# Kernel optimization log

Hardware: AMD Instinct MI355X
Metric: run time of the kernel (lower is better)

The kernel has to match this reference:

```python
import jax, jax.numpy as jnp
import numpy as np

B, S, D, H, F, L, V = 8, 512, 768, 12, 3072, 12, 30522
DK = D // H
SCALE = 1.0 / float(np.sqrt(DK))


def _ln(x, g, b, eps):
    mu = jnp.mean(x, -1, keepdims=True)
    var = jnp.mean((x - mu) ** 2, -1, keepdims=True)
    return (x - mu) / jnp.sqrt(var + eps) * g + b


def setup_inputs() -> dict:
    key = jax.random.key(0)
    ks = jax.random.split(key, 16)
    s = 0.02
    d = {
        'input_ids': jax.random.randint(ks[0], (B, S), 0, V),
        'token_type_ids': jax.random.randint(ks[1], (B, S), 0, 2),
        'attention_mask': jnp.ones((B, S), jnp.float32),
        'word_emb': jax.random.normal(ks[2], (V, D), jnp.float32) * s,
        'pos_emb': jax.random.normal(ks[3], (512, D), jnp.float32) * s,
        'type_emb': jax.random.normal(ks[4], (2, D), jnp.float32) * s,
        'emb_ln_g': jnp.ones((D,), jnp.float32),
        'emb_ln_b': jnp.zeros((D,), jnp.float32),
        # per-layer stacked params (torch Linear convention: W is [out,in])
        'Wq': jax.random.normal(ks[5], (L, D, D), jnp.float32) * s,
        'bq': jnp.zeros((L, D), jnp.float32),
        'Wk': jax.random.normal(ks[6], (L, D, D), jnp.float32) * s,
        'bk': jnp.zeros((L, D), jnp.float32),
        'Wv': jax.random.normal(ks[7], (L, D, D), jnp.float32) * s,
        'bv': jnp.zeros((L, D), jnp.float32),
        'Wo': jax.random.normal(ks[8], (L, D, D), jnp.float32) * s,
        'bo': jnp.zeros((L, D), jnp.float32),
        'attn_ln_g': jnp.ones((L, D), jnp.float32),
        'attn_ln_b': jnp.zeros((L, D), jnp.float32),
        'W1': jax.random.normal(ks[9], (L, F, D), jnp.float32) * s,
        'b1': jnp.zeros((L, F), jnp.float32),
        'W2': jax.random.normal(ks[10], (L, D, F), jnp.float32) * s,
        'b2': jnp.zeros((L, D), jnp.float32),
        'ffn_ln_g': jnp.ones((L, D), jnp.float32),
        'ffn_ln_b': jnp.zeros((L, D), jnp.float32),
    }
    return d


def reference(input_ids, token_type_ids, attention_mask, word_emb, pos_emb,
              type_emb, emb_ln_g, emb_ln_b, Wq, bq, Wk, bk, Wv, bv, Wo, bo,
              attn_ln_g, attn_ln_b, W1, b1, W2, b2, ffn_ln_g, ffn_ln_b):
    # Embeddings (dropout = identity in eval)
    x = word_emb[input_ids] + type_emb[token_type_ids] + pos_emb[:S][None]
    x = _ln(x, emb_ln_g, emb_ln_b, 1e-12)

    mask0 = attention_mask[:, None, None, :] == 0  # (B,1,1,S)

    def step(x, p):
        wq, bq_, wk, bk_, wv, bv_, wo, bo_, ag, ab, w1, b1_, w2, b2_, fg, fb = p
        q = (jnp.einsum('bsd,ed->bse', x, wq) + bq_).reshape(B, S, H, DK).transpose(0, 2, 1, 3)
        k = (jnp.einsum('bsd,ed->bse', x, wk) + bk_).reshape(B, S, H, DK).transpose(0, 2, 1, 3)
        v = (jnp.einsum('bsd,ed->bse', x, wv) + bv_).reshape(B, S, H, DK).transpose(0, 2, 1, 3)
        attn = jnp.einsum('bhqd,bhkd->bhqk', q, k) * SCALE  # (B,H,S,S)
        attn = jnp.where(mask0, -1e9, attn)
        p_attn = jax.nn.softmax(attn, axis=-1)
        ctx = jnp.einsum('bhqk,bhkd->bhqd', p_attn, v).transpose(0, 2, 1, 3).reshape(B, S, D)
        a = _ln(jnp.einsum('bsd,ed->bse', ctx, wo) + bo_ + x, ag, ab, 1e-5)
        # FFN: NO activation, and final LN has NO residual (faithful to source)
        h = jnp.einsum('bsd,fd->bsf', a, w1) + b1_
        y = jnp.einsum('bsf,df->bsd', h, w2) + b2_
        return _ln(y, fg, fb, 1e-5), None

    x, _ = jax.lax.scan(step, x, (Wq, bq, Wk, bk, Wv, bv, Wo, bo,
                                  attn_ln_g, attn_ln_b, W1, b1, W2, b2,
                                  ffn_ln_g, ffn_ln_b))
    return x
```

## Files before the change

### kernel.cpp

```cpp
#include <hip/hip_runtime.h>
#include <hip/hip_bf16.h>
#include <cstdint>
#include <cstddef>

typedef __bf16 bf16;
typedef __bf16 bf16x8 __attribute__((ext_vector_type(8)));
typedef __bf16 bf16x4 __attribute__((ext_vector_type(4)));
typedef float  floatx4 __attribute__((ext_vector_type(4)));

__device__ __forceinline__ void gload_lds16(const bf16* g, bf16* l) {
    __builtin_amdgcn_global_load_lds((const __attribute__((address_space(1))) void*)g,
                                     (__attribute__((address_space(3))) void*)l, 16, 0, 0);
}

__device__ __forceinline__ floatx4 mfma16(bf16x8 a, bf16x8 b, floatx4 c) {
    return __builtin_amdgcn_mfma_f32_16x16x32_bf16(a, b, c, 0, 0, 0);
}

template<int MODE, int TN, int SPLITK>
__global__ __launch_bounds__(256)
void gemm_bt(const bf16* __restrict__ A, const bf16* __restrict__ Bw,
             const float* __restrict__ bias0, const float* __restrict__ bias1,
             const float* __restrict__ bias2,
             float* __restrict__ Cf, float* __restrict__ Cf1,
             bf16* __restrict__ Cb0, bf16* __restrict__ Cb1,
             bf16* __restrict__ Cb2,
             int M, int N, int K)
{
    constexpr int NJ  = TN / 32;
    constexpr int ASZ = 128 * 32;
    constexpr int BSZ = TN * 32;
    __shared__ __attribute__((aligned(16))) bf16 As[2 * ASZ];
    __shared__ __attribute__((aligned(16))) bf16 Bs[2 * BSZ];

    const int tid  = threadIdx.x;
    const int lane = tid & 63;
    const int wv   = tid >> 6;
    const int quad = lane >> 4;
    const int l16  = lane & 15;

    int bx = blockIdx.x, by = blockIdx.y;
    {
        const int nwg = gridDim.x * gridDim.y;
        if ((nwg & 7) == 0) {
            int wg = by * gridDim.x + bx;
            wg = (wg & 7) * (nwg >> 3) + (wg >> 3);
            bx = wg % gridDim.x;
            by = wg / gridDim.x;
        }
    }
    const int m0 = by * 128;
    const int n0 = bx * TN;
    const int wm = wv & 1;
    const int wn = wv >> 1;

    const int kz   = (SPLITK > 1) ? blockIdx.z : 0;
    const int Ksub = K / SPLITK;

    floatx4 acc[4][NJ] = {};

    const int srow = lane >> 2;
    const int scol = (lane & 3) * 8;
    const bf16* gA0 = A  + (size_t)(m0 + wv * 16 + srow) * K + kz * Ksub + scol;
    const bf16* gA1 = gA0 + (size_t)64 * K;
    const bf16* gB0 = Bw + (size_t)(n0 + wv * 16 + srow) * K + kz * Ksub + scol;
    const bf16* gB1 = gB0 + (size_t)64 * K;
    bf16* lA0 = &As[wv * 512];
    bf16* lA1 = &As[2048 + wv * 512];
    bf16* lB0 = &Bs[wv * 512];
    bf16* lB1 = &Bs[2048 + wv * 512];

    auto stage = [&](int k0, int bi) {
        gload_lds16(gA0 + k0, lA0 + bi * ASZ);
        gload_lds16(gA1 + k0, lA1 + bi * ASZ);
        gload_lds16(gB0 + k0, lB0 + bi * BSZ);
        if (TN == 128) gload_lds16(gB1 + k0, lB1 + bi * BSZ);
    };

    stage(0, 0);
    int cur = 0;
    for (int k0 = 0; k0 < Ksub; k0 += 32) {
        __syncthreads();
        if (k0 + 32 < Ksub) stage(k0 + 32, cur ^ 1);

        const bf16* Ab = &As[cur * ASZ];
        const bf16* Bb = &Bs[cur * BSZ];
        bf16x8 af[4], bfr[NJ];
        #pragma unroll
        for (int i = 0; i < 4; ++i)
            af[i] = *(const bf16x8*)&Ab[(wm * 64 + i * 16 + l16) * 32 + quad * 8];
        #pragma unroll
        for (int j = 0; j < NJ; ++j)
            bfr[j] = *(const bf16x8*)&Bb[(wn * NJ * 16 + j * 16 + l16) * 32 + quad * 8];

        #pragma unroll
        for (int i = 0; i < 4; ++i)
            #pragma unroll
            for (int j = 0; j < NJ; ++j)
                acc[i][j] = mfma16(af[i], bfr[j], acc[i][j]);
        cur ^= 1;
    }

    float* dstF = (SPLITK > 1 && kz != 0) ? Cf1 : Cf;

    #pragma unroll
    for (int i = 0; i < 4; ++i) {
        const int rbase = m0 + wm * 64 + i * 16 + quad * 4;
        #pragma unroll
        for (int j = 0; j < NJ; ++j) {
            const int col = n0 + wn * NJ * 16 + j * 16 + l16;
            if (MODE == 0) {
                const float bv = (SPLITK > 1 && kz != 0) ? 0.f : bias0[col];
                #pragma unroll
                for (int r = 0; r < 4; ++r)
                    dstF[(size_t)(rbase + r) * N + col] = acc[i][j][r] + bv;
            } else if (MODE == 1) {
                const float bv = bias0[col];
                #pragma unroll
                for (int r = 0; r < 4; ++r)
                    Cb0[(size_t)(rbase + r) * N + col] = (bf16)(acc[i][j][r] + bv);
            } else {
                const int sel = col / 768;
                const int cc  = col - sel * 768;
                if (sel < 2) {
                    bf16* dst = (sel == 0) ? Cb0 : Cb1;
                    const float bv = ((sel == 0) ? bias0 : bias1)[cc];
                    #pragma unroll
                    for (int r = 0; r < 4; ++r)
                        dst[(size_t)(rbase + r) * 768 + cc] = (bf16)(acc[i][j][r] + bv);
                } else {
                    const float bv = bias2[cc];
                    const int bb = rbase >> 9, s = rbase & 511;
                    const int h = cc >> 6, d = cc & 63;
                    bf16x4 o;
                    #pragma unroll
                    for (int r = 0; r < 4; ++r) o[r] = (bf16)(acc[i][j][r] + bv);
                    *(bf16x4*)(Cb2 + (((size_t)(bb * 12 + h) * 64 + d) * 512 + s)) = o;
                }
            }
        }
    }
}

__global__ __launch_bounds__(256)
void cvt_all(const float* __restrict__ Wq, const float* __restrict__ Wk,
             const float* __restrict__ Wv, const float* __restrict__ Wo,
             const float* __restrict__ W1, const float* __restrict__ W2,
             bf16* __restrict__ out)
{
    const int l = blockIdx.y;
    const size_t i = ((size_t)blockIdx.x * 256 + threadIdx.x) * 4;
    const size_t wdd = 589824, wdf = 2359296;
    const float* src;
    size_t off;
    if      (i <  589824) { src = Wq + l * wdd; off = i; }
    else if (i < 1179648) { src = Wk + l * wdd; off = i - 589824; }
    else if (i < 1769472) { src = Wv + l * wdd; off = i - 1179648; }
    else if (i < 2359296) { src = Wo + l * wdd; off = i - 1769472; }
    else if (i < 4718592) { src = W1 + l * wdf; off = i - 2359296; }
    else                  { src = W2 + l * wdf; off = i - 4718592; }
    const float4 v = *(const float4*)(src + off);
    bf16x4 o;
    o[0] = (bf16)v.x; o[1] = (bf16)v.y; o[2] = (bf16)v.z; o[3] = (bf16)v.w;
    *(bf16x4*)(out + (size_t)l * 7077888 + i) = o;
}

__global__ __launch_bounds__(256)
void attn3(const bf16* __restrict__ Q, const bf16* __restrict__ Kb,
           const bf16* __restrict__ VT, const float* __restrict__ mask,
           bf16* __restrict__ CTX)
{
    __shared__ __attribute__((aligned(16))) bf16 Ks[2][64 * 64];
    __shared__ __attribute__((aligned(16))) bf16 Vs[2][64 * 64];
    __shared__ __attribute__((aligned(16))) bf16 Ps[4 * 16 * 72];
    __shared__ float mb[512];

    const int tid  = threadIdx.x;
    const int lane = tid & 63;
    const int w    = tid >> 6;
    const int quad = lane >> 4;
    const int l16  = lane & 15;
    const int qt = blockIdx.x, h = blockIdx.y, b = blockIdx.z;

    mb[tid]       = (mask[b * 512 + tid] == 0.f)       ? -1e9f : -16.0f;
    mb[tid + 256] = (mask[b * 512 + tid + 256] == 0.f) ? -1e9f : -16.0f;

    bf16x8 qf0, qf1;
    {
        const bf16* qp = Q + (size_t)(b * 512 + qt * 64 + w * 16 + l16) * 768 + h * 64;
        qf0 = *(const bf16x8*)(qp + quad * 8);
        qf1 = *(const bf16x8*)(qp + 32 + quad * 8);
    }

    float lsum[4] = {0.f, 0.f, 0.f, 0.f};
    floatx4 accO[4] = {};
    bf16* pw = &Ps[w * 1152];

    const int srow8 = lane >> 3;
    const int scol8 = ((lane & 7) * 8) ^ (srow8 << 3);
    const int r0b   = w * 16;

    auto stageKV = [&](int kt, int bi) {
        #pragma unroll
        for (int i = 0; i < 2; ++i) {
            const int r0 = r0b + i * 8;
            gload_lds16(Kb + (size_t)(b * 512 + kt * 64 + r0 + srow8) * 768 + h * 64 + scol8,
                        &Ks[bi][r0 * 64]);
            gload_lds16(VT + ((size_t)(b * 12 + h) * 64 + r0 + srow8) * 512 + kt * 64 + scol8,
                        &Vs[bi][r0 * 64]);
        }
    };

    stageKV(0, 0);
    int cur = 0;
    const int swm = (l16 & 7) << 3;

    for (int kt = 0; kt < 8; ++kt) {
        __syncthreads();
        if (kt < 7) stageKV(kt + 1, cur ^ 1);

        #pragma unroll
        for (int ct = 0; ct < 4; ++ct) {
            const bf16x8 kf0 = *(const bf16x8*)&Ks[cur][(ct * 16 + l16) * 64 + ((quad * 8) ^ swm)];
            const bf16x8 kf1 = *(const bf16x8*)&Ks[cur][(ct * 16 + l16) * 64 + ((quad * 8 + 32) ^ swm)];
            floatx4 a = {0.f, 0.f, 0.f, 0.f};
            a = mfma16(qf0, kf0, a);
            a = mfma16(qf1, kf1, a);
            const float mbv = mb[kt * 64 + ct * 16 + l16];
            #pragma unroll
            for (int r = 0; r < 4; ++r) {
                const float p = __expf(fmaf(a[r], 0.125f, mbv));
                lsum[r] += p;
                pw[(quad * 4 + r) * 72 + ct * 16 + l16] = (bf16)p;
            }
        }

        #pragma unroll
        for (int kc = 0; kc < 2; ++kc) {
            const bf16x8 af = *(const bf16x8*)&pw[l16 * 72 + kc * 32 + quad * 8];
            #pragma unroll
            for (int ct2 = 0; ct2 < 4; ++ct2) {
                const bf16x8 bv = *(const bf16x8*)&Vs[cur][(ct2 * 16 + l16) * 64 + ((kc * 32 + quad * 8) ^ swm)];
                accO[ct2] = mfma16(af, bv, accO[ct2]);
            }
        }
        cur ^= 1;
    }

    float inv[4];
    #pragma unroll
    for (int r = 0; r < 4; ++r) {
        float s = lsum[r];
        #pragma unroll
        for (int o = 1; o < 16; o <<= 1) s += __shfl_xor(s, o);
        inv[r] = 1.0f / s;
    }
    #pragma unroll
    for (int ct2 = 0; ct2 < 4; ++ct2)
        #pragma unroll
        for (int r = 0; r < 4; ++r) {
            const int row = qt * 64 + w * 16 + quad * 4 + r;
            CTX[(size_t)(b * 512 + row) * 768 + h * 64 + ct2 * 16 + l16] =
                (bf16)(accO[ct2][r] * inv[r]);
        }
}

__global__ __launch_bounds__(256)
void embed_ln_k(const int* __restrict__ ids, const int* __restrict__ tts,
                const float* __restrict__ we, const float* __restrict__ pe,
                const float* __restrict__ te, const float* __restrict__ g,
                const float* __restrict__ b, float* __restrict__ X,
                bf16* __restrict__ XB)
{
    __shared__ float red[4];
    const int row = blockIdx.x;
    const int s   = row & 511;
    const int tid = threadIdx.x;
    const int id  = ids[row];
    const int tt  = tts[row];
    const float* pwp = we + (size_t)id * 768;
    const float* pt = te + (size_t)tt * 768;
    const float* pp = pe + (size_t)s * 768;
    const size_t base = (size_t)row * 768;

    float v[3];
    #pragma unroll
    for (int j = 0; j < 3; ++j) {
        const int c = tid + j * 256;
        v[j] = pwp[c] + pt[c] + pp[c];
    }
    float sm = v[0] + v[1] + v[2];
    for (int o = 32; o; o >>= 1) sm += __shfl_down(sm, o);
    if ((tid & 63) == 0) red[tid >> 6] = sm;
    __syncthreads();
    const float mu = (red[0] + red[1] + red[2] + red[3]) * (1.0f / 768.0f);
    float q = 0.f;
    #pragma unroll
    for (int j = 0; j < 3; ++j) { const float d = v[j] - mu; q += d * d; }
    __syncthreads();
    for (int o = 32; o; o >>= 1) q += __shfl_down(q, o);
    if ((tid & 63) == 0) red[tid >> 6] = q;
    __syncthreads();
    const float var  = (red[0] + red[1] + red[2] + red[3]) * (1.0f / 768.0f);
    const float rstd = rsqrtf(var + 1e-12f);
    #pragma unroll
    for (int j = 0; j < 3; ++j) {
        const int c = tid + j * 256;
        const float o = (v[j] - mu) * rstd * g[c] + b[c];
        X[base + c]  = o;
        XB[base + c] = (bf16)o;
    }
}

__global__ __launch_bounds__(256)
void ln_k(const float* T, const float* T2, const float* res,
          const float* g, const float* bta,
          float* Xo, bf16* XBo)
{
    __shared__ float red[4];
    const int row = blockIdx.x;
    const int tid = threadIdx.x;
    const size_t base = (size_t)row * 768;

    float v[3];
    #pragma unroll
    for (int j = 0; j < 3; ++j) {
        const int c = tid + j * 256;
        float x = T[base + c];
        if (T2)  x += T2[base + c];
        if (res) x += res[base + c];
        v[j] = x;
    }
    float sm = v[0] + v[1] + v[2];
    for (int o = 32; o; o >>= 1) sm += __shfl_down(sm, o);
    if ((tid & 63) == 0) red[tid >> 6] = sm;
    __syncthreads();
    const float mu = (red[0] + red[1] + red[2] + red[3]) * (1.0f / 768.0f);
    float q = 0.f;
    #pragma unroll
    for (int j = 0; j < 3; ++j) { const float d = v[j] - mu; q += d * d; }
    __syncthreads();
    for (int o = 32; o; o >>= 1) q += __shfl_down(q, o);
    if ((tid & 63) == 0) red[tid >> 6] = q;
    __syncthreads();
    const float var  = (red[0] + red[1] + red[2] + red[3]) * (1.0f / 768.0f);
    const float rstd = rsqrtf(var + 1e-5f);
    #pragma unroll
    for (int j = 0; j < 3; ++j) {
        const int c = tid + j * 256;
        const float o = (v[j] - mu) * rstd * g[c] + bta[c];
        Xo[base + c]  = o;
        XBo[base + c] = (bf16)o;
    }
}

extern "C" void kernel_launch(void* const* d_in, const int* in_sizes, int n_in,
                              void* d_out, int out_size, void* d_ws, size_t ws_size,
                              hipStream_t stream)
{
    const int*   ids  = (const int*)d_in[0];
    const int*   tts  = (const int*)d_in[1];
    const float* mask = (const float*)d_in[2];
    const float* wemb = (const float*)d_in[3];
    const float* pemb = (const float*)d_in[4];
    const float* temb = (const float*)d_in[5];
    const float* eg   = (const float*)d_in[6];
    const float* eb   = (const float*)d_in[7];
    const float* Wq   = (const float*)d_in[8];
    const float* bq   = (const float*)d_in[9];
    const float* Wk   = (const float*)d_in[10];
    const float* bk   = (const float*)d_in[11];
    const float* Wv   = (const float*)d_in[12];
    const float* bv   = (const float*)d_in[13];
    const float* Wo   = (const float*)d_in[14];
    const float* bo   = (const float*)d_in[15];
    const float* ag   = (const float*)d_in[16];
    const float* ab   = (const float*)d_in[17];
    const float* W1   = (const float*)d_in[18];
    const float* b1   = (const float*)d_in[19];
    const float* W2   = (const float*)d_in[20];
    const float* b2   = (const float*)d_in[21];
    const float* fg   = (const float*)d_in[22];
    const float* fb   = (const float*)d_in[23];

    char* p = (char*)d_ws;
    float* X   = (float*)p; p += 12582912;
    bf16* XB   = (bf16*)p;  p += 6291456;
    bf16* Qb   = (bf16*)p;  p += 6291456;
    bf16* Kbuf = (bf16*)p;  p += 6291456;
    bf16* CTXb = (bf16*)p;  p += 6291456;
    float* T1  = (float*)p; p += 12582912;
    bf16* HB   = (bf16*)p;  p += 25165824;
    bf16* WB   = (bf16*)p;  p += 169869312;
    bf16* VT   = HB;
    float* T1b = (float*)Qb;

    cvt_all<<<dim3(6912, 12), 256, 0, stream>>>(Wq, Wk, Wv, Wo, W1, W2, WB);
    embed_ln_k<<<4096, 256, 0, stream>>>(ids, tts, wemb, pemb, temb, eg, eb, X, XB);

    for (int l = 0; l < 12; ++l) {
        bf16* wb = WB + (size_t)l * 7077888;
        gemm_bt<2, 128, 1><<<dim3(18, 32), 256, 0, stream>>>(
            XB, wb, bq + l * 768, bk + l * 768, bv + l * 768,
            nullptr, nullptr, Qb, Kbuf, VT, 4096, 2304, 768);
        attn3<<<dim3(8, 12, 8), 256, 0, stream>>>(Qb, Kbuf, VT, mask, CTXb);
        gemm_bt<0, 64, 2><<<dim3(12, 32, 2), 256, 0, stream>>>(
            CTXb, wb + 1769472, bo + l * 768, nullptr, nullptr,
            T1, T1b, nullptr, nullptr, nullptr, 4096, 768, 768);
        ln_k<<<4096, 256, 0, stream>>>(T1, T1b, X, ag + l * 768, ab + l * 768, X, XB);
        gemm_bt<1, 128, 1><<<dim3(24, 32), 256, 0, stream>>>(
            XB, wb + 2359296, b1 + (size_t)l * 3072, nullptr, nullptr,
            nullptr, nullptr, HB, nullptr, nullptr, 4096, 3072, 768);
        gemm_bt<0, 64, 2><<<dim3(12, 32, 2), 256, 0, stream>>>(
            HB, wb + 4718592, b2 + l * 768, nullptr, nullptr,
            T1, T1b, nullptr, nullptr, nullptr, 4096, 768, 3072);
        float* outX = (l == 11) ? (float*)d_out : X;
        ln_k<<<4096, 256, 0, stream>>>(T1, T1b, nullptr, fg + l * 768, fb + l * 768, outX, XB);
    }
}
```

Baseline: 2.330 ms.

## Triple-buffer GEMM LDS staging with vmcnt waits; coarsen weight conversion kernel

The GEMM main loop moves from a double-buffered LDS pipeline with __syncthreads to a three-stage ring. Loads are issued two K-steps ahead, and an explicit s_waitcnt vmcnt plus s_barrier waits only for the oldest stage, so global-to-LDS copies overlap more with MFMA work. The weight-conversion kernel now has each thread handle four float4 chunks with a quarter of the blocks, cutting launch and scheduling overhead. The larger LDS footprint may lower occupancy, and the hand-written vmcnt counts depend on how many loads each stage issues.

Result: no change. 2.315 ms (-0.7%).

```diff
diff --git a/kernel.cpp b/kernel.cpp
--- a/kernel.cpp
+++ b/kernel.cpp
@@ -30,8 +30,8 @@
     constexpr int NJ  = TN / 32;
     constexpr int ASZ = 128 * 32;
     constexpr int BSZ = TN * 32;
-    __shared__ __attribute__((aligned(16))) bf16 As[2 * ASZ];
-    __shared__ __attribute__((aligned(16))) bf16 Bs[2 * BSZ];
+    __shared__ __attribute__((aligned(16))) bf16 As[3 * ASZ];
+    __shared__ __attribute__((aligned(16))) bf16 Bs[3 * BSZ];
 
     const int tid  = threadIdx.x;
     const int lane = tid & 63;
@@ -77,14 +77,9 @@
         if (TN == 128) gload_lds16(gB1 + k0, lB1 + bi * BSZ);
     };
 
-    stage(0, 0);
-    int cur = 0;
-    for (int k0 = 0; k0 < Ksub; k0 += 32) {
-        __syncthreads();
-        if (k0 + 32 < Ksub) stage(k0 + 32, cur ^ 1);
-
-        const bf16* Ab = &As[cur * ASZ];
-        const bf16* Bb = &Bs[cur * BSZ];
+    auto compute = [&](int bi) {
+        const bf16* Ab = &As[bi * ASZ];
+        const bf16* Bb = &Bs[bi * BSZ];
         bf16x8 af[4], bfr[NJ];
         #pragma unroll
         for (int i = 0; i < 4; ++i)
@@ -92,14 +87,31 @@
         #pragma unroll
         for (int j = 0; j < NJ; ++j)
             bfr[j] = *(const bf16x8*)&Bb[(wn * NJ * 16 + j * 16 + l16) * 32 + quad * 8];
-
         #pragma unroll
         for (int i = 0; i < 4; ++i)
             #pragma unroll
             for (int j = 0; j < NJ; ++j)
                 acc[i][j] = mfma16(af[i], bfr[j], acc[i][j]);
-        cur ^= 1;
-    }
+    };
+
+    stage(0, 0);
+    stage(32, 1);
+    int cur = 0;
+    int k0  = 0;
+    for (; k0 < Ksub - 32; k0 += 32) {
+        if constexpr (TN == 128) asm volatile("s_waitcnt vmcnt(4)" ::: "memory");
+        else                     asm volatile("s_waitcnt vmcnt(3)" ::: "memory");
+        __builtin_amdgcn_s_barrier();
+        if (k0 + 64 < Ksub) {
+            int b2 = cur + 2; if (b2 >= 3) b2 -= 3;
+            stage(k0 + 64, b2);
+        }
+        compute(cur);
+        if (++cur == 3) cur = 0;
+    }
+    asm volatile("s_waitcnt vmcnt(0)" ::: "memory");
+    __builtin_amdgcn_s_barrier();
+    compute(cur);
 
     float* dstF = (SPLITK > 1 && kz != 0) ? Cf1 : Cf;
 
@@ -149,20 +161,23 @@
              bf16* __restrict__ out)
 {
     const int l = blockIdx.y;
-    const size_t i = ((size_t)blockIdx.x * 256 + threadIdx.x) * 4;
     const size_t wdd = 589824, wdf = 2359296;
-    const float* src;
-    size_t off;
-    if      (i <  589824) { src = Wq + l * wdd; off = i; }
-    else if (i < 1179648) { src = Wk + l * wdd; off = i - 589824; }
-    else if (i < 1769472) { src = Wv + l * wdd; off = i - 1179648; }
-    else if (i < 2359296) { src = Wo + l * wdd; off = i - 1769472; }
-    else if (i < 4718592) { src = W1 + l * wdf; off = i - 2359296; }
-    else                  { src = W2 + l * wdf; off = i - 4718592; }
-    const float4 v = *(const float4*)(src + off);
-    bf16x4 o;
-    o[0] = (bf16)v.x; o[1] = (bf16)v.y; o[2] = (bf16)v.z; o[3] = (bf16)v.w;
-    *(bf16x4*)(out + (size_t)l * 7077888 + i) = o;
+    #pragma unroll
+    for (int j = 0; j < 4; ++j) {
+        const size_t i = (((size_t)blockIdx.x * 4 + j) * 256 + threadIdx.x) * 4;
+        const float* src;
+        size_t off;
+        if      (i <  589824) { src = Wq + l * wdd; off = i; }
+        else if (i < 1179648) { src = Wk + l * wdd; off = i - 589824; }
+        else if (i < 1769472) { src = Wv + l * wdd; off = i - 1179648; }
+        else if (i < 2359296) { src = Wo + l * wdd; off = i - 1769472; }
+        else if (i < 4718592) { src = W1 + l * wdf; off = i - 2359296; }
+        else                  { src = W2 + l * wdf; off = i - 4718592; }
+        const float4 v = *(const float4*)(src + off);
+        bf16x4 o;
+        o[0] = (bf16)v.x; o[1] = (bf16)v.y; o[2] = (bf16)v.z; o[3] = (bf16)v.w;
+        *(bf16x4*)(out + (size_t)l * 7077888 + i) = o;
+    }
 }
 
 __global__ __launch_bounds__(256)
@@ -395,7 +410,7 @@
     bf16* VT   = HB;
     float* T1b = (float*)Qb;
 
-    cvt_all<<<dim3(6912, 12), 256, 0, stream>>>(Wq, Wk, Wv, Wo, W1, W2, WB);
+    cvt_all<<<dim3(1728, 12), 256, 0, stream>>>(Wq, Wk, Wv, Wo, W1, W2, WB);
     embed_ln_k<<<4096, 256, 0, stream>>>(ids, tts, wemb, pemb, temb, eg, eb, X, XB);
 
     for (int l = 0; l < 12; ++l) {
```
